# Kernel tuning notes

Hardware: AMD Instinct MI355X
Metric: run time of the kernel (lower is better)

## Reference

```python
import jax, jax.numpy as jnp
import numpy as np

B, N, CT, CS, CP, H, NB = 1, 1024, 768, 384, 16, 16, 4
DH = CT // H
NL, NK = 8, 32          # n_local_tokens, n_keys
K = NL + NK
SCALE = 1.0 / np.sqrt(DH)


def _ln(x, g=None, b=None, eps=1e-5):
    m = jnp.mean(x, -1, keepdims=True)
    v = jnp.var(x, -1, keepdims=True)
    y = (x - m) * jax.lax.rsqrt(v + eps)
    if g is not None:
        y = y * g
    if b is not None:
        y = y + b
    return y


def _adaln(a, s, sln_g, sw, sb, shw):
    # AF3 AdaLN: a <- sigmoid(Lin(s_n)) * LN(a) + LinNoBias(s_n)
    an = _ln(a)
    sn = _ln(s, sln_g)
    return jax.nn.sigmoid(sn @ sw + sb) * an + sn @ shw


def _indices(X_L):
    # n_local sequence neighbours (clamped window) + n_keys spatial nearest
    off = jnp.arange(NL) - NL // 2
    loc = jnp.clip(jnp.arange(N)[:, None] + off[None, :], 0, N - 1)  # [N,NL]
    d2 = jnp.sum((X_L[:, :, None, :] - X_L[:, None, :, :]) ** 2, -1)  # [B,N,N]
    _, nk = jax.lax.top_k(-d2, NK)                                    # [B,N,NK]
    loc = jnp.broadcast_to(loc[None], (X_L.shape[0], N, NL))
    return jnp.concatenate([loc, nk], -1)                             # [B,N,K]


def setup_inputs() -> dict:
    key = jax.random.key(0)
    ks = list(jax.random.split(key, 24))
    f32 = jnp.float32

    def rn(k, shape, s=0.02):
        return (jax.random.normal(k, shape) * s).astype(f32)

    d = {}
    d['A_I'] = jax.random.normal(ks[0], (B, N, CT), f32)
    d['S_I'] = jax.random.normal(ks[1], (B, N, CS), f32)
    d['Z_II'] = jax.random.normal(ks[2], (B, N, N, CP), f32)
    d['X_L'] = jax.random.normal(ks[3], (B, N, 3), f32) * 10.0
    d['f'] = jax.random.randint(ks[4], (B, N), 0, 4)
    # attention-pair-bias block params (stacked over NB blocks)
    d['aln1_sln_g'] = jnp.ones((NB, CS), f32)
    d['aln1_sw'] = rn(ks[5], (NB, CS, CT))
    d['aln1_sb'] = jnp.zeros((NB, CT), f32)
    d['aln1_shw'] = rn(ks[6], (NB, CS, CT))
    d['Wq'] = rn(ks[7], (NB, CT, CT))
    d['bq'] = jnp.zeros((NB, CT), f32)
    d['Wk'] = rn(ks[8], (NB, CT, CT))
    d['Wv'] = rn(ks[9], (NB, CT, CT))
    d['pair_ln_g'] = jnp.ones((NB, CP), f32)
    d['pair_ln_b'] = jnp.zeros((NB, CP), f32)
    d['Wb'] = rn(ks[10], (NB, CP, H))
    d['Wg'] = rn(ks[11], (NB, CT, CT))
    d['Wo'] = rn(ks[12], (NB, CT, CT))
    d['sg_w'] = rn(ks[13], (NB, CS, CT))
    d['sg_b'] = jnp.full((NB, CT), -2.0, f32)   # LinearBiasInit(-2.0)
    # conditioned transition block params
    d['aln2_sln_g'] = jnp.ones((NB, CS), f32)
    d['aln2_sw'] = rn(ks[14], (NB, CS, CT))
    d['aln2_sb'] = jnp.zeros((NB, CT), f32)
    d['aln2_shw'] = rn(ks[15], (NB, CS, CT))
    d['t_w1'] = rn(ks[16], (NB, CT, 2 * CT))
    d['t_w2'] = rn(ks[17], (NB, CT, 2 * CT))
    d['t_w3'] = rn(ks[18], (NB, 2 * CT, CT))
    d['tsg_w'] = rn(ks[19], (NB, CS, CT))
    d['tsg_b'] = jnp.full((NB, CT), -2.0, f32)
    return d


def reference(A_I, S_I, Z_II, X_L, f,
              aln1_sln_g, aln1_sw, aln1_sb, aln1_shw,
              Wq, bq, Wk, Wv, pair_ln_g, pair_ln_b, Wb, Wg, Wo, sg_w, sg_b,
              aln2_sln_g, aln2_sw, aln2_sb, aln2_shw,
              t_w1, t_w2, t_w3, tsg_w, tsg_b):
    idx = _indices(X_L)                       # [B,N,K] int
    bb = jnp.arange(B)[:, None, None]
    nn_ = jnp.arange(N)[None, :, None]
    zg = Z_II[bb, nn_, idx]                   # [B,N,K,CP] gathered pair reps
    A = A_I
    for i in range(NB):
        # LocalAttentionPairBias
        an = _adaln(A, S_I, aln1_sln_g[i], aln1_sw[i], aln1_sb[i], aln1_shw[i])
        q = (an @ Wq[i] + bq[i]).reshape(B, N, H, DH)
        kg = (an @ Wk[i])[bb, idx].reshape(B, N, K, H, DH)
        vg = (an @ Wv[i])[bb, idx].reshape(B, N, K, H, DH)
        bias = _ln(zg, pair_ln_g[i], pair_ln_b[i]) @ Wb[i]      # [B,N,K,H]
        sc = jnp.einsum('bnhd,bnkhd->bnhk', q, kg) * SCALE + jnp.swapaxes(bias, -1, -2)
        w = jax.nn.softmax(sc, -1)                               # [B,N,H,K]
        o = jnp.einsum('bnhk,bnkhd->bnhd', w, vg).reshape(B, N, CT)
        o = jax.nn.sigmoid(an @ Wg[i]) * o                       # per-channel gate
        o = jax.nn.sigmoid(S_I @ sg_w[i] + sg_b[i]) * (o @ Wo[i])
        A = A + o                                                # dropout=0 (eval)
        # ConditionedTransitionBlock (SwiGLU, n=2)
        an2 = _adaln(A, S_I, aln2_sln_g[i], aln2_sw[i], aln2_sb[i], aln2_shw[i])
        hb = jax.nn.silu(an2 @ t_w1[i]) * (an2 @ t_w2[i])
        A = A + jax.nn.sigmoid(S_I @ tsg_w[i] + tsg_b[i]) * (hb @ t_w3[i])
    return A
```

## Files before the change

### kernel.cpp

```cpp
#include <hip/hip_runtime.h>
#include <hip/hip_bf16.h>
#include <math.h>
#include <stdint.h>

#define NTOK 1024
#define CT   768
#define CS   384
#define CP   16
#define NH   16
#define DH   48
#define NBLK 4
#define NL   8
#define NKEY 32
#define KTOT 40
#define SCALE_ 0.14433756729740643f

#define WS_BLK      8257536
#define OFF_A1SW    0
#define OFF_A1SHW   294912
#define OFF_QKVG    589824
#define OFF_WO      2949120
#define OFF_SGT     3538944
#define OFF_A2SW    4128768
#define OFF_A2SHW   4423680
#define OFF_TW1     4718592
#define OFF_TW2     5898240
#define OFF_TW3     7077888

typedef __attribute__((ext_vector_type(8))) short short8;
typedef __attribute__((ext_vector_type(4))) float f32x4;

#define AS1 __attribute__((address_space(1)))
#define AS3 __attribute__((address_space(3)))

__device__ __forceinline__ float sigmoidf_(float x) {
    return 1.0f / (1.0f + __expf(-x));
}
__device__ __forceinline__ float bf2f(unsigned short u) {
    union { unsigned int i; float f; } v; v.i = (unsigned int)u << 16; return v.f;
}
__device__ __forceinline__ unsigned short f2bf(float f) {
    return __bfloat16_as_ushort(__float2bfloat16(f));
}

__device__ __forceinline__ void gl_lds16(const void* g, void* l) {
    __builtin_amdgcn_global_load_lds((const AS1 void*)(uintptr_t)g,
                                     (AS3 void*)(uintptr_t)l, 16, 0, 0);
}

struct PrepArgs {
    const float* X_L; int* idx;
    const float* S; const float* g1; const float* g2;
    __hip_bfloat16* S_bf; __hip_bfloat16* snb;
    const float* bq; const float* sg_b; const float* tsg_b;
    float* qb; float* sb2;
};

__global__ __launch_bounds__(384)
void prep_kernel(PrepArgs pa) {
    __shared__ float ls[12];
    const int t = threadIdx.x;
    const int b = blockIdx.x;

    if (b < 256) {
        const int w = t >> 6;
        if (w >= 4) return;
        const int l = t & 63;
        const int n = b * 4 + w;
        const float* X = pa.X_L;
        int* idx = pa.idx;

        const float x0 = X[n * 3 + 0], x1 = X[n * 3 + 1], x2 = X[n * 3 + 2];
        float d[16];
        unsigned long long lkey = ~0ull;
#pragma unroll
        for (int j = 0; j < 16; ++j) {
            int m = j * 64 + l;
            float dx = x0 - X[m * 3 + 0];
            float dy = x1 - X[m * 3 + 1];
            float dz = x2 - X[m * 3 + 2];
            float v = dx * dx + dy * dy + dz * dz;
            d[j] = v;
            unsigned long long key =
                ((unsigned long long)__float_as_uint(v) << 32) | (unsigned int)m;
            lkey = key < lkey ? key : lkey;
        }
        if (l < NL) {
            int loc = n + l - NL / 2;
            loc = loc < 0 ? 0 : (loc > NTOK - 1 ? NTOK - 1 : loc);
            idx[n * KTOT + l] = loc;
        }
        for (int it = 0; it < NKEY; ++it) {
            unsigned long long rk = lkey;
#pragma unroll
            for (int s = 32; s > 0; s >>= 1) {
                unsigned long long o = __shfl_xor(rk, s, 64);
                rk = o < rk ? o : rk;
            }
            unsigned int win = (unsigned int)rk;
            if (l == 0) idx[n * KTOT + NL + it] = (int)win;
            if ((int)(win & 63) == l) {
                int jw = (int)(win >> 6);
                unsigned long long nk = ~0ull;
#pragma unroll
                for (int j = 0; j < 16; ++j) {
                    if (j == jw) d[j] = INFINITY;
                    unsigned long long key =
                        ((unsigned long long)__float_as_uint(d[j]) << 32) |
                        (unsigned int)(j * 64 + l);
                    nk = key < nk ? key : nk;
                }
                lkey = nk;
            }
        }
        return;
    }

    if (b < 1280) {
        int r = b - 256;
        int wid = t >> 6, l = t & 63;
        float v = pa.S[r * CS + t];
        float s = v;
#pragma unroll
        for (int m = 32; m > 0; m >>= 1) s += __shfl_xor(s, m, 64);
        if (l == 0) ls[wid] = s;
        __syncthreads();
        float mean = (ls[0] + ls[1] + ls[2] + ls[3] + ls[4] + ls[5]) * (1.0f / CS);
        float d = v - mean;
        float q = d * d;
#pragma unroll
        for (int m = 32; m > 0; m >>= 1) q += __shfl_xor(q, m, 64);
        if (l == 0) ls[6 + wid] = q;
        __syncthreads();
        float rstd = rsqrtf((ls[6] + ls[7] + ls[8] + ls[9] + ls[10] + ls[11]) *
                            (1.0f / CS) + 1e-5f);
        float ln = d * rstd;
        pa.S_bf[r * CS + t] = __float2bfloat16(v);
#pragma unroll
        for (int j = 0; j < 8; ++j) {
            const float* g = ((j & 1) ? pa.g2 : pa.g1) + (j >> 1) * CS;
            pa.snb[((size_t)j * NTOK + r) * CS + t] = __float2bfloat16(ln * g[t]);
        }
        return;
    }

    {
        int tt = (b - 1280) * 384 + t;
        if (tt < NBLK * 3072) {
            int i = tt / 3072, c = tt % 3072;
            pa.qb[tt] = (c < 768) ? pa.bq[i * 768 + c] : 0.0f;
        }
        if (tt < NBLK * 1536) {
            int i = tt / 1536, c = tt % 1536;
            pa.sb2[tt] = (c < 768) ? pa.sg_b[i * 768 + c] : pa.tsg_b[i * 768 + c - 768];
        }
    }
}

__global__ __launch_bounds__(256)
void adaapply_kernel(const float* __restrict__ A,
                     const __hip_bfloat16* __restrict__ SIG,
                     const __hip_bfloat16* __restrict__ SH,
                     __hip_bfloat16* __restrict__ an) {
    int r = blockIdx.x, t = threadIdx.x;
    int wid = t >> 6, l = t & 63;
    __shared__ float ls[8];
    const float* ar = A + (size_t)r * CT;
    float v0 = ar[t], v1 = ar[t + 256], v2 = ar[t + 512];
    float s = v0 + v1 + v2;
#pragma unroll
    for (int m = 32; m > 0; m >>= 1) s += __shfl_xor(s, m, 64);
    if (l == 0) ls[wid] = s;
    __syncthreads();
    float mean = (ls[0] + ls[1] + ls[2] + ls[3]) * (1.0f / CT);
    float d0 = v0 - mean, d1 = v1 - mean, d2 = v2 - mean;
    float q = d0 * d0 + d1 * d1 + d2 * d2;
#pragma unroll
    for (int m = 32; m > 0; m >>= 1) q += __shfl_xor(q, m, 64);
    if (l == 0) ls[4 + wid] = q;
    __syncthreads();
    float rstd = rsqrtf((ls[4] + ls[5] + ls[6] + ls[7]) * (1.0f / CT) + 1e-5f);
    size_t base = (size_t)r * CT;
    float dd[3] = {d0, d1, d2};
#pragma unroll
    for (int k = 0; k < 3; ++k) {
        int c = t + k * 256;
        float sg = sigmoidf_(__bfloat162float(SIG[base + c]));
        float sh = __bfloat162float(SH[base + c]);
        an[base + c] = __float2bfloat16(sg * dd[k] * rstd + sh);
    }
}

struct ConvDesc { const float* src; __hip_bfloat16* dst; int K; int N; int tstart; int srcStride; };
struct ConvTable { ConvDesc e[14]; };

__global__ __launch_bounds__(256)
void convT_kernel(ConvTable tab) {
    int b = blockIdx.x;
    int ei = 0;
#pragma unroll
    for (int j = 1; j < 14; ++j) if (b >= tab.e[j].tstart) ei = j;
    ConvDesc d = tab.e[ei];
    const float* src = d.src + (size_t)blockIdx.y * d.srcStride;
    unsigned short* dst = (unsigned short*)(d.dst + (size_t)blockIdx.y * WS_BLK);
    int tt = b - d.tstart;
    int ntn = d.N / 128;
    int k0 = (tt / ntn) * 128, n0 = (tt % ntn) * 128;

    const int ck = threadIdx.x & 15;
    const int cn = threadIdx.x >> 4;

    const float* sp = src + (size_t)(k0 + ck * 8) * d.N + n0 + cn * 8;
    f32x4 va[8], vb[8];
#pragma unroll
    for (int r = 0; r < 8; ++r) {
        va[r] = *(const f32x4*)(sp + (size_t)r * d.N);
        vb[r] = *(const f32x4*)(sp + (size_t)r * d.N + 4);
    }
    unsigned short* dp = dst + (size_t)(n0 + cn * 8) * d.K + k0 + ck * 8;
#pragma unroll
    for (int j = 0; j < 8; ++j) {
        short8 o;
#pragma unroll
        for (int e = 0; e < 8; ++e) {
            float f = (j < 4) ? va[e][j] : vb[e][j - 4];
            o[e] = (short)f2bf(f);
        }
        *(short8*)(dp + (size_t)j * d.K) = o;
    }
}

template <int MODE>
__global__ __launch_bounds__(256)
void gemmw_kernel(const __hip_bfloat16* A, const __hip_bfloat16* B1,
                  const float* cb1, const float* cb2,
                  __hip_bfloat16* outb, __hip_bfloat16* outb2,
                  int K, int N, int ldo) {
    __shared__ __align__(16) char As[2][16384];
    __shared__ __align__(16) char Bs[2][8192];

    const float* cb = cb1;
    __hip_bfloat16* outp = outb;
    if constexpr (MODE == 5) {
        int z = blockIdx.z;
        int j = z & 7, half = z >> 3;
        A += (size_t)j * NTOK * CS;
        B1 += (size_t)(j >> 1) * WS_BLK + ((j & 1) ? OFF_A2SW : OFF_A1SW)
            + (size_t)half * (OFF_A1SHW - OFF_A1SW);
        cb = half ? nullptr : (((j & 1) ? cb2 : cb1) + (j >> 1) * CT);
        outp = (half ? outb2 : outb) + (size_t)j * NTOK * CT;
    } else if constexpr (MODE == 6) {
        int z = blockIdx.z;
        B1 += (size_t)z * WS_BLK;
        cb = cb1 + z * 1536;
        outp = outb + (size_t)z * NTOK * 1536;
    }

    const int tid = threadIdx.x;
    const int lane = tid & 63;
    const int wid = tid >> 6;
    const int row0 = blockIdx.y * 128;
    const int col0 = blockIdx.x * 64;

    const int srow = tid >> 3;
    const int sg_e = (((tid & 7) ^ (srow & 7)) << 3);
    const __hip_bfloat16* ag = A + (size_t)(row0 + srow) * K + sg_e;
    const __hip_bfloat16* bg = B1 + (size_t)(col0 + srow) * K + sg_e;
    const size_t r32K = (size_t)32 * K;

    auto STAGE = [&](int bi) {
        char* al = As[bi] + tid * 16;
        char* bl = Bs[bi] + tid * 16;
        gl_lds16(ag, al);
        gl_lds16(ag + r32K, al + 4096);
        gl_lds16(ag + 2 * r32K, al + 8192);
        gl_lds16(ag + 3 * r32K, al + 12288);
        gl_lds16(bg, bl);
        gl_lds16(bg + r32K, bl + 4096);
        ag += 64; bg += 64;
    };

    f32x4 acc[2][4];
#pragma unroll
    for (int i = 0; i < 2; ++i)
#pragma unroll
        for (int j = 0; j < 4; ++j) acc[i][j] = (f32x4){0.f, 0.f, 0.f, 0.f};

    const int l15 = lane & 15;
    const int lhi = lane >> 4;
    const int nIter = K >> 6;

    STAGE(0);
    for (int it = 0; it < nIter; ++it) {
        __syncthreads();
        if (it + 1 < nIter) STAGE((it + 1) & 1);
        const char* Ab = As[it & 1];
        const char* Bb = Bs[it & 1];
#pragma unroll
        for (int kk = 0; kk < 2; ++kk) {
            const int c = lhi + 4 * kk;
            short8 a[2], bv[4];
#pragma unroll
            for (int mi = 0; mi < 2; ++mi) {
                int ra = wid * 32 + mi * 16 + l15;
                a[mi] = *(const short8*)(Ab + ra * 128 + (((c ^ (ra & 7)) << 4)));
            }
#pragma unroll
            for (int ni = 0; ni < 4; ++ni) {
                int rb = ni * 16 + l15;
                bv[ni] = *(const short8*)(Bb + rb * 128 + (((c ^ (rb & 7)) << 4)));
            }
#pragma unroll
            for (int mi = 0; mi < 2; ++mi)
#pragma unroll
                for (int ni = 0; ni < 4; ++ni)
                    acc[mi][ni] = __builtin_amdgcn_mfma_f32_16x16x32_bf16(
                        a[mi], bv[ni], acc[mi][ni], 0, 0, 0);
        }
    }

#pragma unroll
    for (int mi = 0; mi < 2; ++mi)
#pragma unroll
        for (int ni = 0; ni < 4; ++ni) {
            int col = col0 + ni * 16 + l15;
            int rbase = row0 + wid * 32 + mi * 16 + lhi * 4;
            float cbv = cb ? cb[col] : 0.0f;
            f32x4 v = acc[mi][ni];
#pragma unroll
            for (int r = 0; r < 4; ++r)
                outp[(size_t)(rbase + r) * ldo + col] = __float2bfloat16(v[r] + cbv);
        }
}

template <int MODE>
__global__ __launch_bounds__(256)
void gemm_kernel(const __hip_bfloat16* __restrict__ A,
                 const __hip_bfloat16* B1,
                 const __hip_bfloat16* B2,
                 const __hip_bfloat16* __restrict__ auxb, int ld_aux,
                 float* __restrict__ outf,
                 __hip_bfloat16* outb,
                 int K, int N, int ldo) {
    constexpr bool DUAL = (MODE == 2);
    __shared__ __align__(16) char As[2][8192];
    __shared__ __align__(16) char Bs[2][8192];
    __shared__ __align__(16) char Bs2[DUAL ? 2 : 1][DUAL ? 8192 : 16];

    const int tid = threadIdx.x;
    const int lane = tid & 63;
    const int wid = tid >> 6;
    const int wr = wid >> 1, wc = wid & 1;
    const int row0 = blockIdx.y * 64;
    const int col0 = blockIdx.x * 64;

    const int srow = tid >> 3;
    const int sg_e = (((tid & 7) ^ (srow & 7)) << 3);
    const __hip_bfloat16* ag = A + (size_t)(row0 + srow) * K + sg_e;
    const __hip_bfloat16* bg = B1 + (size_t)(col0 + srow) * K + sg_e;
    const __hip_bfloat16* bg2 = DUAL ? (B2 + (size_t)(col0 + srow) * K + sg_e) : nullptr;
    const size_t r32K = (size_t)32 * K;

    auto STAGE = [&](int bi) {
        gl_lds16(ag, As[bi] + tid * 16);
        gl_lds16(ag + r32K, As[bi] + 4096 + tid * 16);
        gl_lds16(bg, Bs[bi] + tid * 16);
        gl_lds16(bg + r32K, Bs[bi] + 4096 + tid * 16);
        if (DUAL) {
            gl_lds16(bg2, Bs2[bi] + tid * 16);
            gl_lds16(bg2 + r32K, Bs2[bi] + 4096 + tid * 16);
            bg2 += 64;
        }
        ag += 64; bg += 64;
    };

    f32x4 acc[2][2];
    f32x4 acc2[2][2];
#pragma unroll
    for (int i = 0; i < 2; ++i)
#pragma unroll
        for (int j = 0; j < 2; ++j) {
            acc[i][j] = (f32x4){0.f, 0.f, 0.f, 0.f};
            acc2[i][j] = (f32x4){0.f, 0.f, 0.f, 0.f};
        }

    const int l15 = lane & 15;
    const int lhi = lane >> 4;
    const int nIter = K >> 6;

    STAGE(0);
    for (int it = 0; it < nIter; ++it) {
        __syncthreads();
        if (it + 1 < nIter) STAGE((it + 1) & 1);
        const char* Ab = As[it & 1];
        const char* Bb = Bs[it & 1];
        const char* Cb = DUAL ? Bs2[it & 1] : nullptr;
#pragma unroll
        for (int kk = 0; kk < 2; ++kk) {
            const int c = lhi + 4 * kk;
            const int ra0 = wr * 32 + l15, ra1 = ra0 + 16;
            const int rb0 = wc * 32 + l15, rb1 = rb0 + 16;
            short8 a0 = *(const short8*)(Ab + ra0 * 128 + (((c ^ (ra0 & 7)) << 4)));
            short8 a1 = *(const short8*)(Ab + ra1 * 128 + (((c ^ (ra1 & 7)) << 4)));
            short8 b0 = *(const short8*)(Bb + rb0 * 128 + (((c ^ (rb0 & 7)) << 4)));
            short8 b1 = *(const short8*)(Bb + rb1 * 128 + (((c ^ (rb1 & 7)) << 4)));
            acc[0][0] = __builtin_amdgcn_mfma_f32_16x16x32_bf16(a0, b0, acc[0][0], 0, 0, 0);
            acc[0][1] = __builtin_amdgcn_mfma_f32_16x16x32_bf16(a0, b1, acc[0][1], 0, 0, 0);
            acc[1][0] = __builtin_amdgcn_mfma_f32_16x16x32_bf16(a1, b0, acc[1][0], 0, 0, 0);
            acc[1][1] = __builtin_amdgcn_mfma_f32_16x16x32_bf16(a1, b1, acc[1][1], 0, 0, 0);
            if (DUAL) {
                short8 c0 = *(const short8*)(Cb + rb0 * 128 + (((c ^ (rb0 & 7)) << 4)));
                short8 c1 = *(const short8*)(Cb + rb1 * 128 + (((c ^ (rb1 & 7)) << 4)));
                acc2[0][0] = __builtin_amdgcn_mfma_f32_16x16x32_bf16(a0, c0, acc2[0][0], 0, 0, 0);
                acc2[0][1] = __builtin_amdgcn_mfma_f32_16x16x32_bf16(a0, c1, acc2[0][1], 0, 0, 0);
                acc2[1][0] = __builtin_amdgcn_mfma_f32_16x16x32_bf16(a1, c0, acc2[1][0], 0, 0, 0);
                acc2[1][1] = __builtin_amdgcn_mfma_f32_16x16x32_bf16(a1, c1, acc2[1][1], 0, 0, 0);
            }
        }
    }

#pragma unroll
    for (int mi = 0; mi < 2; ++mi)
#pragma unroll
        for (int ni = 0; ni < 2; ++ni) {
            f32x4 v1 = acc[mi][ni];
            f32x4 v2 = acc2[mi][ni];
            int col = col0 + wc * 32 + ni * 16 + l15;
            int rbase = row0 + wr * 32 + mi * 16 + lhi * 4;
#pragma unroll
            for (int r = 0; r < 4; ++r) {
                int row = rbase + r;
                size_t o = (size_t)row * ldo + col;
                if (MODE == 2) {
                    float x = v1[r];
                    outb[o] = __float2bfloat16(x * sigmoidf_(x) * v2[r]);
                } else {
                    float g = sigmoidf_(__bfloat162float(auxb[(size_t)row * ld_aux + col]));
                    outf[o] += g * v1[r];
                }
            }
        }
}

__global__ __launch_bounds__(256)
void attn_kernel(const __hip_bfloat16* __restrict__ qkvg,
                 const float* __restrict__ Z,
                 const int* __restrict__ idx,
                 const float* __restrict__ pg, const float* __restrict__ pb,
                 const float* __restrict__ Wbp,
                 __hip_bfloat16* __restrict__ o2) {
    int n = blockIdx.x;
    int t = threadIdx.x;
    __shared__ __align__(16) unsigned short qs[768];
    __shared__ float sc[16][48];
    __shared__ float lnz[KTOT][16];
    __shared__ float wb[16][17];
    __shared__ float pgs[16], pbs[16];
    __shared__ int sidx[KTOT];
    __shared__ float pacc[96][8];

    wb[t >> 4][t & 15] = Wbp[t];
    if (t < 96) ((short8*)qs)[t] = ((const short8*)(qkvg + (size_t)n * 3072))[t];
    if (t >= 96 && t < 96 + KTOT) sidx[t - 96] = idx[n * KTOT + (t - 96)];
    if (t >= 160 && t < 176) pgs[t - 160] = pg[t - 160];
    if (t >= 176 && t < 192) pbs[t - 176] = pb[t - 176];
    __syncthreads();

    if (t < KTOT) {
        const f32x4* z = (const f32x4*)(Z + ((size_t)n * NTOK + sidx[t]) * CP);
        f32x4 z0 = z[0], z1 = z[1], z2 = z[2], z3 = z[3];
        float v[16];
#pragma unroll
        for (int e = 0; e < 4; ++e) { v[e] = z0[e]; v[4 + e] = z1[e]; v[8 + e] = z2[e]; v[12 + e] = z3[e]; }
        float s = 0.0f;
#pragma unroll
        for (int c = 0; c < 16; ++c) s += v[c];
        float mean = s * (1.0f / 16.0f);
        float s2 = 0.0f;
#pragma unroll
        for (int c = 0; c < 16; ++c) { float d = v[c] - mean; s2 += d * d; }
        float rstd = rsqrtf(s2 * (1.0f / 16.0f) + 1e-5f);
#pragma unroll
        for (int c = 0; c < 16; ++c) lnz[t][c] = (v[c] - mean) * rstd * pgs[c] + pbs[c];
    }
    __syncthreads();

    for (int task = t; task < NH * KTOT; task += 256) {
        int h = task / KTOT, k = task - h * KTOT;
        const short8* kp = (const short8*)((const unsigned short*)qkvg +
                                           (size_t)sidx[k] * 3072 + 768 + h * DH);
        const short8* qp = (const short8*)(qs + h * DH);
        float s = 0.0f;
#pragma unroll
        for (int j = 0; j < 6; ++j) {
            short8 kv = kp[j];
            short8 qv = qp[j];
#pragma unroll
            for (int e = 0; e < 8; ++e)
                s += bf2f((unsigned short)qv[e]) * bf2f((unsigned short)kv[e]);
        }
        float bias = 0.0f;
#pragma unroll
        for (int c = 0; c < 16; ++c) bias += lnz[k][c] * wb[c][h];
        sc[h][k] = s * SCALE_ + bias;
    }
    __syncthreads();

    {
        int h = t >> 4, l = t & 15;
        float v0 = sc[h][l];
        float v1 = sc[h][l + 16];
        float v2 = (l < 8) ? sc[h][l + 32] : -INFINITY;
        float mx = fmaxf(fmaxf(v0, v1), v2);
#pragma unroll
        for (int m = 8; m > 0; m >>= 1) mx = fmaxf(mx, __shfl_xor(mx, m, 16));
        float e0 = __expf(v0 - mx), e1 = __expf(v1 - mx);
        float e2 = (l < 8) ? __expf(v2 - mx) : 0.0f;
        float sm = e0 + e1 + e2;
#pragma unroll
        for (int m = 8; m > 0; m >>= 1) sm += __shfl_xor(sm, m, 16);
        float inv = 1.0f / sm;
        sc[h][l] = e0 * inv;
        sc[h][l + 16] = e1 * inv;
        if (l < 8) sc[h][l + 32] = e2 * inv;
    }
    __syncthreads();

    float acc[8] = {0, 0, 0, 0, 0, 0, 0, 0};
    const int half = (t >= 96) ? 1 : 0;
    const int tt = t - half * 96;
    if (t < 192) {
        int h = tt / 6, c6 = tt - h * 6;
        int d0 = c6 * 8;
        const unsigned short* vbase = (const unsigned short*)qkvg + 1536 + h * DH + d0;
        for (int k = half * 20; k < half * 20 + 20; ++k) {
            short8 vv = *(const short8*)(vbase + (size_t)sidx[k] * 3072);
            float w = sc[h][k];
#pragma unroll
            for (int e = 0; e < 8; ++e) acc[e] += w * bf2f((unsigned short)vv[e]);
        }
    }
    if (half && t < 192) {
#pragma unroll
        for (int e = 0; e < 8; ++e) pacc[tt][e] = acc[e];
    }
    __syncthreads();
    if (t < 96) {
        int h = t / 6, c6 = t - h * 6;
        int d0 = c6 * 8;
        short8 gv = *(const short8*)((const unsigned short*)qkvg +
                                     (size_t)n * 3072 + 2304 + h * DH + d0);
        short8 ov;
#pragma unroll
        for (int e = 0; e < 8; ++e) {
            float g = sigmoidf_(bf2f((unsigned short)gv[e]));
            ov[e] = (short)f2bf(g * (acc[e] + pacc[t][e]));
        }
        *(short8*)((unsigned short*)o2 + (size_t)n * CT + h * DH + d0) = ov;
    }
}

extern "C" void kernel_launch(void* const* d_in, const int* in_sizes, int n_in,
                              void* d_out, int out_size, void* d_ws, size_t ws_size,
                              hipStream_t stream) {
    const float* A_I  = (const float*)d_in[0];
    const float* S_I  = (const float*)d_in[1];
    const float* Z_II = (const float*)d_in[2];
    const float* X_L  = (const float*)d_in[3];
    const float* aln1_sln_g = (const float*)d_in[5];
    const float* aln1_sw    = (const float*)d_in[6];
    const float* aln1_sb    = (const float*)d_in[7];
    const float* aln1_shw   = (const float*)d_in[8];
    const float* Wq  = (const float*)d_in[9];
    const float* bq  = (const float*)d_in[10];
    const float* Wk  = (const float*)d_in[11];
    const float* Wv  = (const float*)d_in[12];
    const float* pair_ln_g = (const float*)d_in[13];
    const float* pair_ln_b = (const float*)d_in[14];
    const float* Wbp = (const float*)d_in[15];
    const float* Wg  = (const float*)d_in[16];
    const float* Wo  = (const float*)d_in[17];
    const float* sg_w = (const float*)d_in[18];
    const float* sg_b = (const float*)d_in[19];
    const float* aln2_sln_g = (const float*)d_in[20];
    const float* aln2_sw    = (const float*)d_in[21];
    const float* aln2_sb    = (const float*)d_in[22];
    const float* aln2_shw   = (const float*)d_in[23];
    const float* t_w1 = (const float*)d_in[24];
    const float* t_w2 = (const float*)d_in[25];
    const float* t_w3 = (const float*)d_in[26];
    const float* tsg_w = (const float*)d_in[27];
    const float* tsg_b = (const float*)d_in[28];
    (void)in_sizes; (void)n_in; (void)out_size; (void)ws_size;

    float* A = (float*)d_out;

    char* ws = (char*)d_ws;
    size_t off = 0;
    auto alloc = [&](size_t bytes) {
        void* p = ws + off;
        off += (bytes + 255) & ~(size_t)255;
        return p;
    };
    int*   idx    = (int*)  alloc(NTOK * KTOT * 4);
    __hip_bfloat16* S_bf  = (__hip_bfloat16*)alloc((size_t)NTOK * CS * 2);
    __hip_bfloat16* snb   = (__hip_bfloat16*)alloc((size_t)8 * NTOK * CS * 2);
    __hip_bfloat16* an    = (__hip_bfloat16*)alloc((size_t)NTOK * CT * 2);
    __hip_bfloat16* qkvg  = (__hip_bfloat16*)alloc((size_t)NTOK * 3072 * 2);
    __hip_bfloat16* sgateb= (__hip_bfloat16*)alloc((size_t)NBLK * NTOK * 1536 * 2);
    __hip_bfloat16* SIG   = (__hip_bfloat16*)alloc((size_t)8 * NTOK * CT * 2);
    __hip_bfloat16* SH    = (__hip_bfloat16*)alloc((size_t)8 * NTOK * CT * 2);
    __hip_bfloat16* o2    = (__hip_bfloat16*)alloc((size_t)NTOK * CT * 2);
    __hip_bfloat16* hb    = (__hip_bfloat16*)alloc((size_t)NTOK * 2 * CT * 2);
    float* qkvgbias = (float*)alloc((size_t)NBLK * 3072 * 4);
    float* sgbias   = (float*)alloc((size_t)NBLK * 1536 * 4);
    __hip_bfloat16* Wbuf = (__hip_bfloat16*)alloc((size_t)NBLK * WS_BLK * 2);

    hipMemcpyAsync(A, A_I, (size_t)NTOK * CT * 4, hipMemcpyDeviceToDevice, stream);

    {
        PrepArgs pa;
        pa.X_L = X_L; pa.idx = idx;
        pa.S = S_I; pa.g1 = aln1_sln_g; pa.g2 = aln2_sln_g;
        pa.S_bf = S_bf; pa.snb = snb;
        pa.bq = bq; pa.sg_b = sg_b; pa.tsg_b = tsg_b;
        pa.qb = qkvgbias; pa.sb2 = sgbias;
        prep_kernel<<<1312, 384, 0, stream>>>(pa);
    }

    {
        ConvTable tab;
        int p = 0, ts = 0;
        auto add = [&](const float* s, size_t dstOff, int Kk, int Nn, int sstride) {
            tab.e[p].src = s; tab.e[p].dst = Wbuf + dstOff; tab.e[p].K = Kk;
            tab.e[p].N = Nn; tab.e[p].tstart = ts; tab.e[p].srcStride = sstride;
            ts += (Kk / 128) * (Nn / 128); ++p;
        };
        add(aln1_sw,  OFF_A1SW,           384, 768,  CS * CT);
        add(aln1_shw, OFF_A1SHW,          384, 768,  CS * CT);
        add(Wq, OFF_QKVG + 0 * 589824,    768, 768,  CT * CT);
        add(Wk, OFF_QKVG + 1 * 589824,    768, 768,  CT * CT);
        add(Wv, OFF_QKVG + 2 * 589824,    768, 768,  CT * CT);
        add(Wg, OFF_QKVG + 3 * 589824,    768, 768,  CT * CT);
        add(Wo, OFF_WO,                   768, 768,  CT * CT);
        add(sg_w,  OFF_SGT,               384, 768,  CS * CT);
        add(tsg_w, OFF_SGT + 768 * 384,   384, 768,  CS * CT);
        add(aln2_sw,  OFF_A2SW,           384, 768,  CS * CT);
        add(aln2_shw, OFF_A2SHW,          384, 768,  CS * CT);
        add(t_w1, OFF_TW1,                768, 1536, CT * 2 * CT);
        add(t_w2, OFF_TW2,                768, 1536, CT * 2 * CT);
        add(t_w3, OFF_TW3,                1536, 768, 2 * CT * CT);
        convT_kernel<<<dim3(ts, NBLK), 256, 0, stream>>>(tab);
    }

    gemmw_kernel<5><<<dim3(12, 8, 16), 256, 0, stream>>>(
        snb, Wbuf, aln1_sb, aln2_sb, SIG, SH, 384, 768, 768);
    gemmw_kernel<6><<<dim3(24, 8, 4), 256, 0, stream>>>(
        S_bf, Wbuf + OFF_SGT, sgbias, nullptr, sgateb, nullptr, 384, 1536, 1536);

    for (int i = 0; i < NBLK; ++i) {
        const __hip_bfloat16* Wb_i = Wbuf + (size_t)i * WS_BLK;
        __hip_bfloat16* sg_i = sgateb + (size_t)i * NTOK * 1536;

        adaapply_kernel<<<NTOK, 256, 0, stream>>>(
            A, SIG + (size_t)(2 * i) * NTOK * CT, SH + (size_t)(2 * i) * NTOK * CT, an);
        gemmw_kernel<4><<<dim3(48, 8), 256, 0, stream>>>(
            an, Wb_i + OFF_QKVG, qkvgbias + (size_t)i * 3072, nullptr,
            qkvg, nullptr, 768, 3072, 3072);
        attn_kernel<<<NTOK, 256, 0, stream>>>(
            qkvg, Z_II, idx, pair_ln_g + (size_t)i * CP, pair_ln_b + (size_t)i * CP,
            Wbp + (size_t)i * CP * NH, o2);
        gemm_kernel<3><<<dim3(12, 16), 256, 0, stream>>>(
            o2, Wb_i + OFF_WO, nullptr, sg_i, 1536, A, nullptr, 768, 768, 768);

        adaapply_kernel<<<NTOK, 256, 0, stream>>>(
            A, SIG + (size_t)(2 * i + 1) * NTOK * CT, SH + (size_t)(2 * i + 1) * NTOK * CT, an);
        gemm_kernel<2><<<dim3(24, 16), 256, 0, stream>>>(
            an, Wb_i + OFF_TW1, Wb_i + OFF_TW2, nullptr, 0, nullptr, hb, 768, 1536, 1536);
        gemm_kernel<3><<<dim3(12, 16), 256, 0, stream>>>(
            hb, Wb_i + OFF_TW3, nullptr, sg_i + 768, 1536, A, nullptr, 1536, 768, 768);
    }
}
```

Baseline: 407.7 us.

## Convert fp32 weights to bf16 inside GEMM loads, drop separate transpose pass

Removes the up-front convT kernel that transposed and cast every weight matrix to a bf16 workspace. GEMMs now read the fp32 weights directly, convert them in registers and write them swizzled into LDS. The two hoisted S-projection GEMMs are merged into one launch. The residual GEMMs use a split-K grid of 2 with atomicAdd into A. This saves a full pass over the weights and a workspace, at the cost of reading weights as fp32 (twice the bytes, re-read per row-tile), extra conversion ALU work, and nondeterministic atomic accumulation.

```diff
diff --git a/kernel.cpp b/kernel.cpp
--- a/kernel.cpp
+++ b/kernel.cpp
@@ -15,20 +15,9 @@
 #define KTOT 40
 #define SCALE_ 0.14433756729740643f
 
-#define WS_BLK      8257536
-#define OFF_A1SW    0
-#define OFF_A1SHW   294912
-#define OFF_QKVG    589824
-#define OFF_WO      2949120
-#define OFF_SGT     3538944
-#define OFF_A2SW    4128768
-#define OFF_A2SHW   4423680
-#define OFF_TW1     4718592
-#define OFF_TW2     5898240
-#define OFF_TW3     7077888
-
 typedef __attribute__((ext_vector_type(8))) short short8;
 typedef __attribute__((ext_vector_type(4))) float f32x4;
+typedef __attribute__((ext_vector_type(2))) unsigned int u32x2;
 
 #define AS1 __attribute__((address_space(1)))
 #define AS3 __attribute__((address_space(3)))
@@ -191,111 +180,68 @@
     }
 }
 
-struct ConvDesc { const float* src; __hip_bfloat16* dst; int K; int N; int tstart; int srcStride; };
-struct ConvTable { ConvDesc e[14]; };
-
-__global__ __launch_bounds__(256)
-void convT_kernel(ConvTable tab) {
-    int b = blockIdx.x;
-    int ei = 0;
-#pragma unroll
-    for (int j = 1; j < 14; ++j) if (b >= tab.e[j].tstart) ei = j;
-    ConvDesc d = tab.e[ei];
-    const float* src = d.src + (size_t)blockIdx.y * d.srcStride;
-    unsigned short* dst = (unsigned short*)(d.dst + (size_t)blockIdx.y * WS_BLK);
-    int tt = b - d.tstart;
-    int ntn = d.N / 128;
-    int k0 = (tt / ntn) * 128, n0 = (tt % ntn) * 128;
-
-    const int ck = threadIdx.x & 15;
-    const int cn = threadIdx.x >> 4;
-
-    const float* sp = src + (size_t)(k0 + ck * 8) * d.N + n0 + cn * 8;
-    f32x4 va[8], vb[8];
-#pragma unroll
-    for (int r = 0; r < 8; ++r) {
-        va[r] = *(const f32x4*)(sp + (size_t)r * d.N);
-        vb[r] = *(const f32x4*)(sp + (size_t)r * d.N + 4);
-    }
-    unsigned short* dp = dst + (size_t)(n0 + cn * 8) * d.K + k0 + ck * 8;
-#pragma unroll
-    for (int j = 0; j < 8; ++j) {
-        short8 o;
-#pragma unroll
-        for (int e = 0; e < 8; ++e) {
-            float f = (j < 4) ? va[e][j] : vb[e][j - 4];
-            o[e] = (short)f2bf(f);
-        }
-        *(short8*)(dp + (size_t)j * d.K) = o;
-    }
-}
-
-template <int MODE>
-__global__ __launch_bounds__(256)
-void gemmw_kernel(const __hip_bfloat16* A, const __hip_bfloat16* B1,
-                  const float* cb1, const float* cb2,
-                  __hip_bfloat16* outb, __hip_bfloat16* outb2,
-                  int K, int N, int ldo) {
-    __shared__ __align__(16) char As[2][16384];
-    __shared__ __align__(16) char Bs[2][8192];
-
-    const float* cb = cb1;
-    __hip_bfloat16* outp = outb;
-    if constexpr (MODE == 5) {
-        int z = blockIdx.z;
-        int j = z & 7, half = z >> 3;
-        A += (size_t)j * NTOK * CS;
-        B1 += (size_t)(j >> 1) * WS_BLK + ((j & 1) ? OFF_A2SW : OFF_A1SW)
-            + (size_t)half * (OFF_A1SHW - OFF_A1SW);
-        cb = half ? nullptr : (((j & 1) ? cb2 : cb1) + (j >> 1) * CT);
-        outp = (half ? outb2 : outb) + (size_t)j * NTOK * CT;
-    } else if constexpr (MODE == 6) {
-        int z = blockIdx.z;
-        B1 += (size_t)z * WS_BLK;
-        cb = cb1 + z * 1536;
-        outp = outb + (size_t)z * NTOK * 1536;
-    }
-
+__device__ __forceinline__ void wide_body(
+    const __hip_bfloat16* A, int K,
+    const float* W, int Wld,
+    const float* cb, __hip_bfloat16* out, int ldo,
+    int row0, int wcol0, int ocol0,
+    char* As0, char* As1, char* Bs0, char* Bs1) {
     const int tid = threadIdx.x;
     const int lane = tid & 63;
     const int wid = tid >> 6;
-    const int row0 = blockIdx.y * 128;
-    const int col0 = blockIdx.x * 64;
+    char* Asb[2] = {As0, As1};
+    char* Bsb[2] = {Bs0, Bs1};
 
     const int srow = tid >> 3;
     const int sg_e = (((tid & 7) ^ (srow & 7)) << 3);
     const __hip_bfloat16* ag = A + (size_t)(row0 + srow) * K + sg_e;
-    const __hip_bfloat16* bg = B1 + (size_t)(col0 + srow) * K + sg_e;
     const size_t r32K = (size_t)32 * K;
 
-    auto STAGE = [&](int bi) {
-        char* al = As[bi] + tid * 16;
-        char* bl = Bs[bi] + tid * 16;
-        gl_lds16(ag, al);
-        gl_lds16(ag + r32K, al + 4096);
-        gl_lds16(ag + 2 * r32K, al + 8192);
-        gl_lds16(ag + 3 * r32K, al + 12288);
-        gl_lds16(bg, bl);
-        gl_lds16(bg + r32K, bl + 4096);
-        ag += 64; bg += 64;
-    };
-
-    f32x4 acc[2][4];
-#pragma unroll
-    for (int i = 0; i < 2; ++i)
-#pragma unroll
-        for (int j = 0; j < 4; ++j) acc[i][j] = (f32x4){0.f, 0.f, 0.f, 0.f};
+    const int kq = tid >> 4;
+    const int nq = tid & 15;
+    const float* wp = W + (size_t)kq * 4 * Wld + wcol0 + nq * 4;
+    f32x4 breg[4];
 
     const int l15 = lane & 15;
     const int lhi = lane >> 4;
     const int nIter = K >> 6;
 
-    STAGE(0);
+    f32x4 acc[2][4];
+#pragma unroll
+    for (int i = 0; i < 2; ++i)
+#pragma unroll
+        for (int j = 0; j < 4; ++j) acc[i][j] = (f32x4){0.f, 0.f, 0.f, 0.f};
+
+#pragma unroll
+    for (int r = 0; r < 4; ++r) breg[r] = *(const f32x4*)(wp + (size_t)r * Wld);
+    {
+        char* al = Asb[0] + tid * 16;
+        gl_lds16(ag, al); gl_lds16(ag + r32K, al + 4096);
+        gl_lds16(ag + 2 * r32K, al + 8192); gl_lds16(ag + 3 * r32K, al + 12288);
+        ag += 64;
+    }
+#pragma unroll
+    for (int j = 0; j < 4; ++j) {
+        int n = nq * 4 + j;
+        u32x2 v;
+        v[0] = (unsigned int)f2bf(breg[0][j]) | ((unsigned int)f2bf(breg[1][j]) << 16);
+        v[1] = (unsigned int)f2bf(breg[2][j]) | ((unsigned int)f2bf(breg[3][j]) << 16);
+        *(u32x2*)(Bsb[0] + n * 128 + ((((kq >> 1) ^ (n & 7)) << 4)) + (kq & 1) * 8) = v;
+    }
+
     for (int it = 0; it < nIter; ++it) {
         __syncthreads();
-        if (it + 1 < nIter) STAGE((it + 1) & 1);
-        const char* Ab = As[it & 1];
-        const char* Bb = Bs[it & 1];
+        if (it + 1 < nIter) {
+            const float* p = wp + (size_t)(it + 1) * 64 * Wld;
+#pragma unroll
+            for (int r = 0; r < 4; ++r) breg[r] = *(const f32x4*)(p + (size_t)r * Wld);
+            char* al = Asb[(it + 1) & 1] + tid * 16;
+            gl_lds16(ag, al); gl_lds16(ag + r32K, al + 4096);
+            gl_lds16(ag + 2 * r32K, al + 8192); gl_lds16(ag + 3 * r32K, al + 12288);
+            ag += 64;
+        }
+        const char* Ab = Asb[it & 1];
+        const char* Bb = Bsb[it & 1];
 #pragma unroll
         for (int kk = 0; kk < 2; ++kk) {
             const int c = lhi + 4 * kk;
@@ -317,61 +263,144 @@
                     acc[mi][ni] = __builtin_amdgcn_mfma_f32_16x16x32_bf16(
                         a[mi], bv[ni], acc[mi][ni], 0, 0, 0);
         }
+        if (it + 1 < nIter) {
+            char* B = Bsb[(it + 1) & 1];
+#pragma unroll
+            for (int j = 0; j < 4; ++j) {
+                int n = nq * 4 + j;
+                u32x2 v;
+                v[0] = (unsigned int)f2bf(breg[0][j]) | ((unsigned int)f2bf(breg[1][j]) << 16);
+                v[1] = (unsigned int)f2bf(breg[2][j]) | ((unsigned int)f2bf(breg[3][j]) << 16);
+                *(u32x2*)(B + n * 128 + ((((kq >> 1) ^ (n & 7)) << 4)) + (kq & 1) * 8) = v;
+            }
+        }
     }
 
 #pragma unroll
     for (int mi = 0; mi < 2; ++mi)
 #pragma unroll
         for (int ni = 0; ni < 4; ++ni) {
-            int col = col0 + ni * 16 + l15;
+            int col = ocol0 + ni * 16 + l15;
             int rbase = row0 + wid * 32 + mi * 16 + lhi * 4;
             float cbv = cb ? cb[col] : 0.0f;
             f32x4 v = acc[mi][ni];
 #pragma unroll
             for (int r = 0; r < 4; ++r)
-                outp[(size_t)(rbase + r) * ldo + col] = __float2bfloat16(v[r] + cbv);
-        }
-}
-
-template <int MODE>
+                out[(size_t)(rbase + r) * ldo + col] = __float2bfloat16(v[r] + cbv);
+        }
+}
+
+struct HoistArgs {
+    const __hip_bfloat16* snb; const __hip_bfloat16* S_bf;
+    const float* a1sw; const float* a1shw; const float* a2sw; const float* a2shw;
+    const float* sg_w; const float* tsg_w;
+    const float* a1sb; const float* a2sb; const float* sgbias;
+    __hip_bfloat16* SIG; __hip_bfloat16* SH; __hip_bfloat16* sgateb;
+};
+
 __global__ __launch_bounds__(256)
-void gemm_kernel(const __hip_bfloat16* __restrict__ A,
-                 const __hip_bfloat16* B1,
-                 const __hip_bfloat16* B2,
-                 const __hip_bfloat16* __restrict__ auxb, int ld_aux,
-                 float* __restrict__ outf,
-                 __hip_bfloat16* outb,
-                 int K, int N, int ldo) {
-    constexpr bool DUAL = (MODE == 2);
-    __shared__ __align__(16) char As[2][8192];
+void gemmh_kernel(HoistArgs ha) {
+    __shared__ __align__(16) char As[2][16384];
     __shared__ __align__(16) char Bs[2][8192];
-    __shared__ __align__(16) char Bs2[DUAL ? 2 : 1][DUAL ? 8192 : 16];
-
+    int b = blockIdx.x;
+    if (b < 1536) {
+        int z = b / 96, rem = b % 96;
+        int y = rem / 12, x = rem % 12;
+        int j = z & 7, half = z >> 3;
+        const __hip_bfloat16* A = ha.snb + (size_t)j * NTOK * CS;
+        const float* W = (half ? ((j & 1) ? ha.a2shw : ha.a1shw)
+                               : ((j & 1) ? ha.a2sw : ha.a1sw)) + (size_t)(j >> 1) * CS * CT;
+        const float* cb = half ? nullptr : (((j & 1) ? ha.a2sb : ha.a1sb) + (j >> 1) * CT);
+        __hip_bfloat16* out = (half ? ha.SH : ha.SIG) + (size_t)j * NTOK * CT;
+        wide_body(A, CS, W, CT, cb, out, 768, y * 128, x * 64, x * 64,
+                  As[0], As[1], Bs[0], Bs[1]);
+    } else {
+        int b2 = b - 1536;
+        int z = b2 / 192, rem = b2 % 192;
+        int y = rem / 24, x = rem % 24;
+        const float* W = ((x < 12) ? ha.sg_w : ha.tsg_w) + (size_t)z * CS * CT;
+        int wcol0 = (x < 12) ? x * 64 : (x - 12) * 64;
+        wide_body(ha.S_bf, CS, W, CT, ha.sgbias + z * 1536,
+                  ha.sgateb + (size_t)z * NTOK * 1536, 1536,
+                  y * 128, wcol0, x * 64, As[0], As[1], Bs[0], Bs[1]);
+    }
+}
+
+struct QkvgArgs {
+    const __hip_bfloat16* an;
+    const float* Wt[4];
+    const float* cb;
+    __hip_bfloat16* qkvg;
+};
+
+__global__ __launch_bounds__(256)
+void gemmq_kernel(QkvgArgs qa) {
+    __shared__ __align__(16) char As[2][16384];
+    __shared__ __align__(16) char Bs[2][8192];
+    int x = blockIdx.x, y = blockIdx.y;
+    int sel = x / 12;
+    wide_body(qa.an, CT, qa.Wt[sel], CT, qa.cb, qa.qkvg, 3072,
+              y * 128, (x % 12) * 64, x * 64, As[0], As[1], Bs[0], Bs[1]);
+}
+
+template <bool DUAL>
+__device__ __forceinline__ void nar_body(
+    const __hip_bfloat16* A, int Kfull, int Ksub, int koff,
+    const float* W1, const float* W2, int Wld,
+    const __hip_bfloat16* auxb, int ld_aux,
+    float* outf, __hip_bfloat16* outb, int ldo,
+    int row0, int col0,
+    char* As0, char* As1, char* B10, char* B11, char* B20, char* B21) {
     const int tid = threadIdx.x;
     const int lane = tid & 63;
     const int wid = tid >> 6;
     const int wr = wid >> 1, wc = wid & 1;
-    const int row0 = blockIdx.y * 64;
-    const int col0 = blockIdx.x * 64;
+    char* Asb[2] = {As0, As1};
+    char* B1b[2] = {B10, B11};
+    char* B2b[2] = {B20, B21};
 
     const int srow = tid >> 3;
     const int sg_e = (((tid & 7) ^ (srow & 7)) << 3);
-    const __hip_bfloat16* ag = A + (size_t)(row0 + srow) * K + sg_e;
-    const __hip_bfloat16* bg = B1 + (size_t)(col0 + srow) * K + sg_e;
-    const __hip_bfloat16* bg2 = DUAL ? (B2 + (size_t)(col0 + srow) * K + sg_e) : nullptr;
-    const size_t r32K = (size_t)32 * K;
-
-    auto STAGE = [&](int bi) {
-        gl_lds16(ag, As[bi] + tid * 16);
-        gl_lds16(ag + r32K, As[bi] + 4096 + tid * 16);
-        gl_lds16(bg, Bs[bi] + tid * 16);
-        gl_lds16(bg + r32K, Bs[bi] + 4096 + tid * 16);
+    const __hip_bfloat16* ag = A + (size_t)(row0 + srow) * Kfull + koff + sg_e;
+    const size_t r32K = (size_t)32 * Kfull;
+
+    const int kq = tid >> 4;
+    const int nq = tid & 15;
+    const float* wp1 = W1 + (size_t)(koff + kq * 4) * Wld + col0 + nq * 4;
+    const float* wp2 = DUAL ? (W2 + (size_t)(koff + kq * 4) * Wld + col0 + nq * 4) : nullptr;
+    f32x4 b1reg[4], b2reg[4];
+
+    auto BLOAD = [&](int it) {
+        const float* p1 = wp1 + (size_t)it * 64 * Wld;
+#pragma unroll
+        for (int r = 0; r < 4; ++r) b1reg[r] = *(const f32x4*)(p1 + (size_t)r * Wld);
         if (DUAL) {
-            gl_lds16(bg2, Bs2[bi] + tid * 16);
-            gl_lds16(bg2 + r32K, Bs2[bi] + 4096 + tid * 16);
-            bg2 += 64;
-        }
-        ag += 64; bg += 64;
+            const float* p2 = wp2 + (size_t)it * 64 * Wld;
+#pragma unroll
+            for (int r = 0; r < 4; ++r) b2reg[r] = *(const f32x4*)(p2 + (size_t)r * Wld);
+        }
+    };
+    auto BWRITE = [&](int bi) {
+#pragma unroll
+        for (int j = 0; j < 4; ++j) {
+            int n = nq * 4 + j;
+            int boff = n * 128 + ((((kq >> 1) ^ (n & 7)) << 4)) + (kq & 1) * 8;
+            u32x2 v;
+            v[0] = (unsigned int)f2bf(b1reg[0][j]) | ((unsigned int)f2bf(b1reg[1][j]) << 16);
+            v[1] = (unsigned int)f2bf(b1reg[2][j]) | ((unsigned int)f2bf(b1reg[3][j]) << 16);
+            *(u32x2*)(B1b[bi] + boff) = v;
+            if (DUAL) {
+                u32x2 w;
+                w[0] = (unsigned int)f2bf(b2reg[0][j]) | ((unsigned int)f2bf(b2reg[1][j]) << 16);
+                w[1] = (unsigned int)f2bf(b2reg[2][j]) | ((unsigned int)f2bf(b2reg[3][j]) << 16);
+                *(u32x2*)(B2b[bi] + boff) = w;
+            }
+        }
+    };
+    auto ASTAGE = [&](int bi) {
+        gl_lds16(ag, Asb[bi] + tid * 16);
+        gl_lds16(ag + r32K, Asb[bi] + 4096 + tid * 16);
+        ag += 64;
     };
 
     f32x4 acc[2][2];
@@ -386,15 +415,15 @@
 
     const int l15 = lane & 15;
     const int lhi = lane >> 4;
-    const int nIter = K >> 6;
-
-    STAGE(0);
+    const int nIter = Ksub >> 6;
+
+    BLOAD(0); ASTAGE(0); BWRITE(0);
     for (int it = 0; it < nIter; ++it) {
         __syncthreads();
-        if (it + 1 < nIter) STAGE((it + 1) & 1);
-        const char* Ab = As[it & 1];
-        const char* Bb = Bs[it & 1];
-        const char* Cb = DUAL ? Bs2[it & 1] : nullptr;
+        if (it + 1 < nIter) { BLOAD(it + 1); ASTAGE((it + 1) & 1); }
+        const char* Ab = Asb[it & 1];
+        const char* Bb = B1b[it & 1];
+        const char* Cb = DUAL ? B2b[it & 1] : nullptr;
 #pragma unroll
         for (int kk = 0; kk < 2; ++kk) {
             const int c = lhi + 4 * kk;
@@ -417,6 +446,7 @@
                 acc2[1][1] = __builtin_amdgcn_mfma_f32_16x16x32_bf16(a1, c1, acc2[1][1], 0, 0, 0);
             }
         }
+        if (it + 1 < nIter) BWRITE((it + 1) & 1);
     }
 
 #pragma unroll
@@ -431,15 +461,38 @@
             for (int r = 0; r < 4; ++r) {
                 int row = rbase + r;
                 size_t o = (size_t)row * ldo + col;
-                if (MODE == 2) {
+                if (DUAL) {
                     float x = v1[r];
                     outb[o] = __float2bfloat16(x * sigmoidf_(x) * v2[r]);
                 } else {
                     float g = sigmoidf_(__bfloat162float(auxb[(size_t)row * ld_aux + col]));
-                    outf[o] += g * v1[r];
+                    atomicAdd(&outf[o], g * v1[r]);
                 }
             }
         }
+}
+
+__global__ __launch_bounds__(256)
+void gemmd_kernel(const __hip_bfloat16* an, const float* W1, const float* W2,
+                  __hip_bfloat16* hb) {
+    __shared__ __align__(16) char As[2][8192];
+    __shared__ __align__(16) char B1[2][8192];
+    __shared__ __align__(16) char B2[2][8192];
+    nar_body<true>(an, CT, CT, 0, W1, W2, 1536, nullptr, 0, nullptr, hb, 1536,
+                   blockIdx.y * 64, blockIdx.x * 64,
+                   As[0], As[1], B1[0], B1[1], B2[0], B2[1]);
+}
+
+__global__ __launch_bounds__(256)
+void gemmr_kernel(const __hip_bfloat16* Ain, const float* W,
+                  const __hip_bfloat16* auxb, float* Aout,
+                  int Kfull, int Ksub) {
+    __shared__ __align__(16) char As[2][8192];
+    __shared__ __align__(16) char B1[2][8192];
+    nar_body<false>(Ain, Kfull, Ksub, blockIdx.z * Ksub, W, nullptr, 768,
+                    auxb, 1536, Aout, nullptr, 768,
+                    blockIdx.y * 64, blockIdx.x * 64,
+                    As[0], As[1], B1[0], B1[1], nullptr, nullptr);
 }
 
 __global__ __launch_bounds__(256)
@@ -614,7 +667,6 @@
     __hip_bfloat16* hb    = (__hip_bfloat16*)alloc((size_t)NTOK * 2 * CT * 2);
     float* qkvgbias = (float*)alloc((size_t)NBLK * 3072 * 4);
     float* sgbias   = (float*)alloc((size_t)NBLK * 1536 * 4);
-    __hip_bfloat16* Wbuf = (__hip_bfloat16*)alloc((size_t)NBLK * WS_BLK * 2);
 
     hipMemcpyAsync(A, A_I, (size_t)NTOK * CT * 4, hipMemcpyDeviceToDevice, stream);
 
@@ -625,59 +677,46 @@
         pa.S_bf = S_bf; pa.snb = snb;
         pa.bq = bq; pa.sg_b = sg_b; pa.tsg_b = tsg_b;
         pa.qb = qkvgbias; pa.sb2 = sgbias;
-        prep_kernel<<<1312, 384, 0, stream>>>(pa);
+        prep_kernel<<<1328, 384, 0, stream>>>(pa);
     }
 
     {
-        ConvTable tab;
-        int p = 0, ts = 0;
-        auto add = [&](const float* s, size_t dstOff, int Kk, int Nn, int sstride) {
-            tab.e[p].src = s; tab.e[p].dst = Wbuf + dstOff; tab.e[p].K = Kk;
-            tab.e[p].N = Nn; tab.e[p].tstart = ts; tab.e[p].srcStride = sstride;
-            ts += (Kk / 128) * (Nn / 128); ++p;
-        };
-        add(aln1_sw,  OFF_A1SW,           384, 768,  CS * CT);
-        add(aln1_shw, OFF_A1SHW,          384, 768,  CS * CT);
-        add(Wq, OFF_QKVG + 0 * 589824,    768, 768,  CT * CT);
-        add(Wk, OFF_QKVG + 1 * 589824,    768, 768,  CT * CT);
-        add(Wv, OFF_QKVG + 2 * 589824,    768, 768,  CT * CT);
-        add(Wg, OFF_QKVG + 3 * 589824,    768, 768,  CT * CT);
-        add(Wo, OFF_WO,                   768, 768,  CT * CT);
-        add(sg_w,  OFF_SGT,               384, 768,  CS * CT);
-        add(tsg_w, OFF_SGT + 768 * 384,   384, 768,  CS * CT);
-        add(aln2_sw,  OFF_A2SW,           384, 768,  CS * CT);
-        add(aln2_shw, OFF_A2SHW,          384, 768,  CS * CT);
-        add(t_w1, OFF_TW1,                768, 1536, CT * 2 * CT);
-        add(t_w2, OFF_TW2,                768, 1536, CT * 2 * CT);
-        add(t_w3, OFF_TW3,                1536, 768, 2 * CT * CT);
-        convT_kernel<<<dim3(ts, NBLK), 256, 0, stream>>>(tab);
-    }
-
-    gemmw_kernel<5><<<dim3(12, 8, 16), 256, 0, stream>>>(
-        snb, Wbuf, aln1_sb, aln2_sb, SIG, SH, 384, 768, 768);
-    gemmw_kernel<6><<<dim3(24, 8, 4), 256, 0, stream>>>(
-        S_bf, Wbuf + OFF_SGT, sgbias, nullptr, sgateb, nullptr, 384, 1536, 1536);
+        HoistArgs ha;
+        ha.snb = snb; ha.S_bf = S_bf;
+        ha.a1sw = aln1_sw; ha.a1shw = aln1_shw; ha.a2sw = aln2_sw; ha.a2shw = aln2_shw;
+        ha.sg_w = sg_w; ha.tsg_w = tsg_w;
+        ha.a1sb = aln1_sb; ha.a2sb = aln2_sb; ha.sgbias = sgbias;
+        ha.SIG = SIG; ha.SH = SH; ha.sgateb = sgateb;
+        gemmh_kernel<<<2304, 256, 0, stream>>>(ha);
+    }
 
     for (int i = 0; i < NBLK; ++i) {
-        const __hip_bfloat16* Wb_i = Wbuf + (size_t)i * WS_BLK;
         __hip_bfloat16* sg_i = sgateb + (size_t)i * NTOK * 1536;
 
         adaapply_kernel<<<NTOK, 256, 0, stream>>>(
             A, SIG + (size_t)(2 * i) * NTOK * CT, SH + (size_t)(2 * i) * NTOK * CT, an);
-        gemmw_kernel<4><<<dim3(48, 8), 256, 0, stream>>>(
-            an, Wb_i + OFF_QKVG, qkvgbias + (size_t)i * 3072, nullptr,
-            qkvg, nullptr, 768, 3072, 3072);
+        {
+            QkvgArgs qa;
+            qa.an = an;
+            qa.Wt[0] = Wq + (size_t)i * CT * CT;
+            qa.Wt[1] = Wk + (size_t)i * CT * CT;
+            qa.Wt[2] = Wv + (size_t)i * CT * CT;
+            qa.Wt[3] = Wg + (size_t)i * CT * CT;
+            qa.cb = qkvgbias + (size_t)i * 3072;
+            qa.qkvg = qkvg;
+            gemmq_kernel<<<dim3(48, 8), 256, 0, stream>>>(qa);
+        }
         attn_kernel<<<NTOK, 256, 0, stream>>>(
             qkvg, Z_II, idx, pair_ln_g + (size_t)i * CP, pair_ln_b + (size_t)i * CP,
             Wbp + (size_t)i * CP * NH, o2);
-        gemm_kernel<3><<<dim3(12, 16), 256, 0, stream>>>(
-            o2, Wb_i + OFF_WO, nullptr, sg_i, 1536, A, nullptr, 768, 768, 768);
+        gemmr_kernel<<<dim3(12, 16, 2), 256, 0, stream>>>(
+            o2, Wo + (size_t)i * CT * CT, sg_i, A, 768, 384);
 
         adaapply_kernel<<<NTOK, 256, 0, stream>>>(
             A, SIG + (size_t)(2 * i + 1) * NTOK * CT, SH + (size_t)(2 * i + 1) * NTOK * CT, an);
-        gemm_kernel<2><<<dim3(24, 16), 256, 0, stream>>>(
-            an, Wb_i + OFF_TW1, Wb_i + OFF_TW2, nullptr, 0, nullptr, hb, 768, 1536, 1536);
-        gemm_kernel<3><<<dim3(12, 16), 256, 0, stream>>>(
-            hb, Wb_i + OFF_TW3, nullptr, sg_i + 768, 1536, A, nullptr, 1536, 768, 768);
-    }
-}
+        gemmd_kernel<<<dim3(24, 16), 256, 0, stream>>>(
+            an, t_w1 + (size_t)i * CT * 2 * CT, t_w2 + (size_t)i * CT * 2 * CT, hb);
+        gemmr_kernel<<<dim3(12, 16, 2), 256, 0, stream>>>(
+            hb, t_w3 + (size_t)i * 2 * CT * CT, sg_i + 768, A, 1536, 768);
+    }
+}
```

Result: slower. 509.2 us (+24.9%).
